# Kernel tuning notes

Hardware: AMD Instinct MI355X
Metric: run time of the kernel (lower is better)

## Reference

```python
import jax, jax.numpy as jnp
import numpy as np

B, L, HID = 2, 2048, 2048
H, KVH, HD = 8, 1, 256
GROUPS = H // KVH
THETA = 10000.0
NEG_INF = -1e9


def _rope_cos_sin(seq_len, hd):
    inv_freq = 1.0 / (THETA ** (jnp.arange(0, hd, 2, dtype=jnp.float32) / hd))
    t = jnp.arange(seq_len, dtype=jnp.float32)
    freqs = jnp.outer(t, inv_freq)                # [L, hd/2]
    emb = jnp.concatenate([freqs, freqs], axis=-1)  # [L, hd]
    return jnp.cos(emb), jnp.sin(emb)


def _rotate_half(x):
    x1, x2 = jnp.split(x, 2, axis=-1)
    return jnp.concatenate([-x2, x1], axis=-1)


def _apply_rope(x, cos, sin):
    # x: [B, h, L, hd]; cos/sin: [L, hd] broadcast over batch/heads
    return x * cos[None, None] + _rotate_half(x) * sin[None, None]


def setup_inputs() -> dict:
    key = jax.random.key(0)
    kx, kq, kk, kv, ko = jax.random.split(key, 5)
    s = lambda fan_in: 1.0 / np.sqrt(fan_in)
    x = jax.random.normal(kx, (B, L, HID), dtype=jnp.float32)
    Wq = jax.random.normal(kq, (HID, H * HD), dtype=jnp.float32) * s(HID)
    Wk = jax.random.normal(kk, (HID, KVH * HD), dtype=jnp.float32) * s(HID)
    Wv = jax.random.normal(kv, (HID, KVH * HD), dtype=jnp.float32) * s(HID)
    Wo = jax.random.normal(ko, (H * HD, HID), dtype=jnp.float32) * s(H * HD)
    # causal additive mask, same semantics as SDPA attn_mask (float, additive)
    causal = jnp.tril(jnp.ones((L, L), dtype=bool))
    mask = jnp.where(causal, 0.0, NEG_INF).astype(jnp.float32)[None, None]
    return {"x": x, "Wq": Wq, "Wk": Wk, "Wv": Wv, "Wo": Wo, "mask": mask}


def reference(x, Wq, Wk, Wv, Wo, mask):
    # projections -> [B, h, L, hd]
    q = (x @ Wq).reshape(B, L, H, HD).transpose(0, 2, 1, 3)
    k = (x @ Wk).reshape(B, L, KVH, HD).transpose(0, 2, 1, 3)
    v = (x @ Wv).reshape(B, L, KVH, HD).transpose(0, 2, 1, 3)
    cos, sin = _rope_cos_sin(L, HD)
    q = _apply_rope(q, cos, sin)
    k = _apply_rope(k, cos, sin)
    # GQA: replicate kv heads (repeat_interleave over head dim)
    k = jnp.repeat(k, GROUPS, axis=1)
    v = jnp.repeat(v, GROUPS, axis=1)
    scale = HD ** -0.5
    scores = jnp.einsum("bhqd,bhkd->bhqk", q, k) * scale + mask
    attn = jax.nn.softmax(scores.astype(jnp.float32), axis=-1).astype(q.dtype)
    out = jnp.einsum("bhqk,bhkd->bhqd", attn, v)
    out = out.transpose(0, 2, 1, 3).reshape(B, L, H * HD)
    return out @ Wo
```

## Files before the change

### kernel.cpp

```cpp
#include <hip/hip_runtime.h>

typedef unsigned short u16;
typedef __attribute__((ext_vector_type(8))) short short8x;
typedef __attribute__((ext_vector_type(4))) float f32x4;

#define B_ 2
#define L_ 2048
#define HID_ 2048
#define H_ 8
#define HD_ 256

__device__ __forceinline__ u16 f2bf(float f) {
  union { float f; unsigned u; } v; v.f = f;
  unsigned r = v.u + 0x7FFFu + ((v.u >> 16) & 1u);
  return (u16)(r >> 16);
}
__device__ __forceinline__ float bf2f(u16 u) {
  union { unsigned u; float f; } v; v.u = ((unsigned)u) << 16;
  return v.f;
}

__device__ __forceinline__ void gload_lds16(const void* g, void* l) {
  __builtin_amdgcn_global_load_lds((const __attribute__((address_space(1))) unsigned*)g,
                                   (__attribute__((address_space(3))) unsigned*)l, 16, 0, 0);
}

__global__ __launch_bounds__(256) void cvt_x_kernel(const float4* __restrict__ in,
                                                    u16* __restrict__ out) {
  int idx = blockIdx.x * 256 + threadIdx.x;
  float4 v = in[idx];
  u16* o = out + (size_t)idx * 4;
  o[0] = f2bf(v.x); o[1] = f2bf(v.y); o[2] = f2bf(v.z); o[3] = f2bf(v.w);
}

__global__ __launch_bounds__(256) void cvt_wt_kernel(const float* __restrict__ W,
                                                     u16* __restrict__ Wt, int K, int N) {
  __shared__ float tile[32][33];
  int n0 = blockIdx.x * 32, k0 = blockIdx.y * 32;
  int tx = threadIdx.x, ty = threadIdx.y;
#pragma unroll
  for (int i = 0; i < 32; i += 8)
    tile[ty + i][tx] = W[(size_t)(k0 + ty + i) * N + n0 + tx];
  __syncthreads();
#pragma unroll
  for (int i = 0; i < 32; i += 8)
    Wt[(size_t)(n0 + ty + i) * K + k0 + tx] = f2bf(tile[tx][ty + i]);
}

__global__ __launch_bounds__(256) void rope_kernel(const u16* __restrict__ in,
                                                   u16* __restrict__ out, int nh_shift,
                                                   int in_stride, int in_off, float scale) {
  int idx = blockIdx.x * 256 + threadIdx.x;
  int nh = 1 << nh_shift;
  int d = idx & 127;
  int t = idx >> 7;
  int h = t & (nh - 1);
  int row = t >> nh_shift;
  int l = row & (L_ - 1);
  int b = row >> 11;
  size_t ibase = (size_t)row * in_stride + in_off + h * 256 + d;
  float x1 = bf2f(in[ibase]);
  float x2 = bf2f(in[ibase + 128]);
  float f = exp2f(-(float)d * (13.287712379549449f / 128.0f));
  float ang = (float)l * f;
  float s, c;
  sincosf(ang, &s, &c);
  size_t obase = ((size_t)(b * nh + h) * L_ + l) * 256 + d;
  out[obase] = f2bf((x1 * c - x2 * s) * scale);
  out[obase + 128] = f2bf((x2 * c + x1 * s) * scale);
}

__global__ __launch_bounds__(256) void vt_kernel(const u16* __restrict__ qkvproj,
                                                 u16* __restrict__ vt) {
  int idx = blockIdx.x * 256 + threadIdx.x;
  int l = idx & 2047;
  int d = (idx >> 11) & 255;
  int b = idx >> 19;
  vt[idx] = qkvproj[((size_t)b * 2048 + l) * 2560 + 2304 + d];
}

template <int F32OUT>
__global__ __launch_bounds__(256) void gemm_bt_kernel(const u16* __restrict__ A,
                                                      const u16* __restrict__ Bt,
                                                      void* __restrict__ Cv,
                                                      int M, int N, int K) {
  __shared__ __attribute__((aligned(16))) u16 As[128 * 32];
  __shared__ __attribute__((aligned(16))) u16 Bs[128 * 32];
  const int tid = threadIdx.x;
  const int lane = tid & 63;
  const int w = tid >> 6;
  const int wr = w >> 1, wc = w & 1;
  const int nbx = gridDim.x;
  int flat = blockIdx.y * nbx + blockIdx.x;
  int nwg = nbx * gridDim.y;
  int q8 = nwg >> 3, r8 = nwg & 7;
  int xcd = flat & 7, idx8 = flat >> 3;
  int neu = (xcd < r8 ? xcd * (q8 + 1) : r8 * (q8 + 1) + (xcd - r8) * q8) + idx8;
  const int m0 = (neu / nbx) * 128, n0 = (neu % nbx) * 128;
  const int l15 = lane & 15, l4 = lane >> 4;
  f32x4 acc[4][4] = {};
  for (int kt = 0; kt < K; kt += 32) {
#pragma unroll
    for (int i = 0; i < 2; ++i) {
      int c = tid + i * 256;
      int row = c >> 2, cin = c & 3;
      gload_lds16(A + (size_t)(m0 + row) * K + kt + cin * 8,
                  (char*)As + (i * 256 + w * 64) * 16);
      gload_lds16(Bt + (size_t)(n0 + row) * K + kt + cin * 8,
                  (char*)Bs + (i * 256 + w * 64) * 16);
    }
    __syncthreads();
    short8x a[4], b[4];
#pragma unroll
    for (int m = 0; m < 4; ++m)
      a[m] = *(const short8x*)(&As[(wr * 64 + m * 16 + l15) * 32 + l4 * 8]);
#pragma unroll
    for (int n = 0; n < 4; ++n)
      b[n] = *(const short8x*)(&Bs[(wc * 64 + n * 16 + l15) * 32 + l4 * 8]);
#pragma unroll
    for (int m = 0; m < 4; ++m)
#pragma unroll
      for (int n = 0; n < 4; ++n)
        acc[m][n] = __builtin_amdgcn_mfma_f32_16x16x32_bf16(a[m], b[n], acc[m][n], 0, 0, 0);
    __syncthreads();
  }
#pragma unroll
  for (int m = 0; m < 4; ++m) {
#pragma unroll
    for (int n = 0; n < 4; ++n) {
      int gcol = n0 + wc * 64 + n * 16 + l15;
#pragma unroll
      for (int r = 0; r < 4; ++r) {
        int grow = m0 + wr * 64 + m * 16 + l4 * 4 + r;
        if (F32OUT)
          ((float*)Cv)[(size_t)grow * N + gcol] = acc[m][n][r];
        else
          ((u16*)Cv)[(size_t)grow * N + gcol] = f2bf(acc[m][n][r]);
      }
    }
  }
}

__global__ __launch_bounds__(256) void flash_kernel(const u16* __restrict__ qb,
                                                    const u16* __restrict__ kb,
                                                    const u16* __restrict__ vt,
                                                    u16* __restrict__ attn_o) {
  __shared__ __attribute__((aligned(16))) u16 Kbuf[2][64 * 256];
  __shared__ __attribute__((aligned(16))) u16 Vbuf[2][256 * 64];
  __shared__ __attribute__((aligned(16))) u16 Ps[4 * 16 * 64];
  const int x = blockIdx.x;
  const int j = 31 - (x >> 4);
  const int bh = x & 15;
  const int b = bh >> 3;
  const int h = bh & 7;
  const int tid = threadIdx.x, lane = tid & 63, w = tid >> 6;
  const int l15 = lane & 15, l4 = lane >> 4;
  const int q0 = j * 64 + w * 16;
  const int nt = j + 1;

  const u16* qrow = qb + ((size_t)(b * 8 + h) * L_ + q0 + l15) * 256;
  short8x qf[8];
#pragma unroll
  for (int kc = 0; kc < 8; ++kc)
    qf[kc] = *(const short8x*)(qrow + kc * 32 + l4 * 8);

  f32x4 o[16] = {};
  float mrow = -3e38f, srow = 0.f;

  const u16* kbase = kb + (size_t)b * (L_ * 256);
  const u16* vbase = vt + (size_t)b * (256 * L_);

#define STAGE(t, s)                                                            \
  {                                                                            \
    _Pragma("unroll") for (int i2 = 0; i2 < 8; ++i2) {                         \
      int c = i2 * 256 + tid;                                                  \
      int rk = c >> 5, cck = c & 31, jk = cck ^ (rk & 7);                      \
      gload_lds16(kbase + (size_t)((t) * 64 + rk) * 256 + jk * 8,              \
                  (char*)&Kbuf[s][0] + (i2 * 256 + w * 64) * 16);              \
      int rd = c >> 3, ccv = c & 7, jv = ccv ^ (rd & 7);                       \
      gload_lds16(vbase + (size_t)rd * L_ + (t) * 64 + jv * 8,                 \
                  (char*)&Vbuf[s][0] + (i2 * 256 + w * 64) * 16);              \
    }                                                                          \
  }

  STAGE(0, 0);
  asm volatile("s_waitcnt vmcnt(0)" ::: "memory");
  __syncthreads();

  for (int t = 0; t < nt; ++t) {
    if (t + 1 < nt) STAGE(t + 1, (t + 1) & 1);
    const char* Kb = (const char*)&Kbuf[t & 1][0];
    const char* Vb = (const char*)&Vbuf[t & 1][0];

    f32x4 sacc[4] = {};
    __builtin_amdgcn_s_setprio(1);
#pragma unroll
    for (int kc = 0; kc < 8; ++kc)
#pragma unroll
      for (int n = 0; n < 4; ++n) {
        int row = n * 16 + l15;
        short8x kf = *(const short8x*)(Kb +
            ((row * 512 + kc * 64 + l4 * 16) ^ ((row & 7) << 4)));
        sacc[n] = __builtin_amdgcn_mfma_f32_16x16x32_bf16(kf, qf[kc], sacc[n], 0, 0, 0);
      }
    __builtin_amdgcn_s_setprio(0);
    float p[4][4];
    const bool dm = (t == j);
    const int qg = q0 + l15;
    float pm = -3e38f;
#pragma unroll
    for (int n = 0; n < 4; ++n)
#pragma unroll
      for (int r = 0; r < 4; ++r) {
        int kvg = t * 64 + n * 16 + l4 * 4 + r;
        float v = sacc[n][r];
        if (dm && (kvg > qg)) v = -1e30f;
        p[n][r] = v;
        pm = fmaxf(pm, v);
      }
    pm = fmaxf(pm, __shfl_xor(pm, 16));
    pm = fmaxf(pm, __shfl_xor(pm, 32));
    const bool defer = __all(pm <= mrow + 8.f);
    float mn, alpha;
    if (defer) {
      mn = mrow;
    } else {
      mn = fmaxf(mrow, pm);
      alpha = __expf(mrow - mn);
      mrow = mn;
    }
    float rs = 0.f;
#pragma unroll
    for (int n = 0; n < 4; ++n)
#pragma unroll
      for (int r = 0; r < 4; ++r) {
        p[n][r] = __expf(p[n][r] - mn);
        rs += p[n][r];
      }
    rs += __shfl_xor(rs, 16);
    rs += __shfl_xor(rs, 32);
    if (defer) {
      srow += rs;
    } else {
      srow = srow * alpha + rs;
      float av[4];
#pragma unroll
      for (int r = 0; r < 4; ++r)
        av[r] = __shfl(alpha, l4 * 4 + r, 16);
#pragma unroll
      for (int ff = 0; ff < 16; ++ff) {
        o[ff][0] *= av[0]; o[ff][1] *= av[1];
        o[ff][2] *= av[2]; o[ff][3] *= av[3];
      }
    }
#pragma unroll
    for (int n = 0; n < 4; ++n)
#pragma unroll
      for (int r = 0; r < 4; r += 2) {
        unsigned pk;
        asm("v_cvt_pk_bf16_f32 %0, %1, %2" : "=v"(pk) : "v"(p[n][r]), "v"(p[n][r + 1]));
        *(unsigned*)((char*)Ps + w * 2048 +
                     ((l15 * 128 + (n * 16 + l4 * 4 + r) * 2) ^ ((l15 & 7) << 4))) = pk;
      }
    asm volatile("s_waitcnt lgkmcnt(0)" ::: "memory");
    short8x paf[2];
#pragma unroll
    for (int kc2 = 0; kc2 < 2; ++kc2)
      paf[kc2] = *(const short8x*)((const char*)Ps + w * 2048 +
          ((l15 * 128 + kc2 * 64 + l4 * 16) ^ ((l15 & 7) << 4)));
    __builtin_amdgcn_s_setprio(1);
#pragma unroll
    for (int kc2 = 0; kc2 < 2; ++kc2)
#pragma unroll
      for (int ff = 0; ff < 16; ++ff) {
        int rd = ff * 16 + l15;
        short8x vf = *(const short8x*)(Vb +
            ((rd * 128 + kc2 * 64 + l4 * 16) ^ ((rd & 7) << 4)));
        o[ff] = __builtin_amdgcn_mfma_f32_16x16x32_bf16(paf[kc2], vf, o[ff], 0, 0, 0);
      }
    __builtin_amdgcn_s_setprio(0);
    asm volatile("s_waitcnt vmcnt(0)" ::: "memory");
    __syncthreads();
  }
  float sv[4];
#pragma unroll
  for (int r = 0; r < 4; ++r)
    sv[r] = __shfl(srow, l4 * 4 + r, 16);
#pragma unroll
  for (int r = 0; r < 4; ++r) {
    float inv = 1.0f / sv[r];
    int grow = q0 + l4 * 4 + r;
    size_t base = ((size_t)b * L_ + grow) * (size_t)(H_ * HD_) + h * 256;
#pragma unroll
    for (int ff = 0; ff < 16; ++ff)
      attn_o[base + ff * 16 + l15] = f2bf(o[ff][r] * inv);
  }
#undef STAGE
}

extern "C" void kernel_launch(void* const* d_in, const int* in_sizes, int n_in,
                              void* d_out, int out_size, void* d_ws, size_t ws_size,
                              hipStream_t stream) {
  const float* x  = (const float*)d_in[0];
  const float* Wq = (const float*)d_in[1];
  const float* Wk = (const float*)d_in[2];
  const float* Wv = (const float*)d_in[3];
  const float* Wo = (const float*)d_in[4];
  float* out = (float*)d_out;
  char* ws = (char*)d_ws;
  size_t off = 0;
  auto alloc = [&](size_t bytes) {
    void* p = ws + off;
    off = (off + bytes + 255) & ~(size_t)255;
    return p;
  };
  u16* wqkv_t  = (u16*)alloc(2560ull * 2048 * 2);
  u16* wo_t    = (u16*)alloc(2048ull * 2048 * 2);
  u16* xbf     = (u16*)alloc(4096ull * 2048 * 2);
  u16* qkvproj = (u16*)alloc(4096ull * 2560 * 2);
  u16* kb      = (u16*)alloc(4096ull * 256 * 2);
  u16* vtb     = (u16*)alloc(4096ull * 256 * 2);
  u16* qbuf    = xbf;
  u16* attn_o  = qkvproj;

  cvt_x_kernel<<<8192, 256, 0, stream>>>((const float4*)x, xbf);
  cvt_wt_kernel<<<dim3(64, 64), dim3(32, 8), 0, stream>>>(Wq, wqkv_t, 2048, 2048);
  cvt_wt_kernel<<<dim3(8, 64),  dim3(32, 8), 0, stream>>>(Wk, wqkv_t + 2048ull * 2048, 2048, 256);
  cvt_wt_kernel<<<dim3(8, 64),  dim3(32, 8), 0, stream>>>(Wv, wqkv_t + 2304ull * 2048, 2048, 256);
  cvt_wt_kernel<<<dim3(64, 64), dim3(32, 8), 0, stream>>>(Wo, wo_t, 2048, 2048);

  gemm_bt_kernel<0><<<dim3(20, 32), 256, 0, stream>>>(xbf, wqkv_t, qkvproj, 4096, 2560, 2048);

  rope_kernel<<<16384, 256, 0, stream>>>(qkvproj, qbuf, 3, 2560, 0, 0.0625f);
  rope_kernel<<<2048, 256, 0, stream>>>(qkvproj, kb, 0, 2560, 2048, 1.0f);
  vt_kernel<<<4096, 256, 0, stream>>>(qkvproj, vtb);

  flash_kernel<<<512, 256, 0, stream>>>(qbuf, kb, vtb, attn_o);

  gemm_bt_kernel<1><<<dim3(16, 32), 256, 0, stream>>>(attn_o, wo_t, out, 4096, 2048, 2048);
}
```

Measured before the change: 255.1 us.

## Pair causal query tiles per block for balance; tile V transpose through LDS

The flash kernel now runs 512 threads per block. Waves 0-3 handle query tile 31-p and waves 4-7 handle tile p, and both share the staged K/V tiles. The goal is to even out causal-mask work across blocks and halve the grid while reusing each K/V load for two query tiles. In exchange, the short-tile waves sit idle at barriers once their own tile is finished, and the larger block may reduce occupancy. The V transpose kernel also switches to a 32x32 LDS tile so that both its reads and its writes are coalesced.

```diff
diff --git a/kernel.cpp b/kernel.cpp
--- a/kernel.cpp
+++ b/kernel.cpp
@@ -72,11 +72,16 @@
 
 __global__ __launch_bounds__(256) void vt_kernel(const u16* __restrict__ qkvproj,
                                                  u16* __restrict__ vt) {
-  int idx = blockIdx.x * 256 + threadIdx.x;
-  int l = idx & 2047;
-  int d = (idx >> 11) & 255;
-  int b = idx >> 19;
-  vt[idx] = qkvproj[((size_t)b * 2048 + l) * 2560 + 2304 + d];
+  __shared__ u16 tile[32][33];
+  int l0 = blockIdx.x * 32, d0 = blockIdx.y * 32, b = blockIdx.z;
+  int tx = threadIdx.x, ty = threadIdx.y;
+#pragma unroll
+  for (int i = 0; i < 32; i += 8)
+    tile[ty + i][tx] = qkvproj[((size_t)b * 2048 + l0 + ty + i) * 2560 + 2304 + d0 + tx];
+  __syncthreads();
+#pragma unroll
+  for (int i = 0; i < 32; i += 8)
+    vt[((size_t)b * 256 + d0 + ty + i) * 2048 + l0 + tx] = tile[tx][ty + i];
 }
 
 template <int F32OUT>
@@ -141,22 +146,23 @@
   }
 }
 
-__global__ __launch_bounds__(256) void flash_kernel(const u16* __restrict__ qb,
+__global__ __launch_bounds__(512) void flash_kernel(const u16* __restrict__ qb,
                                                     const u16* __restrict__ kb,
                                                     const u16* __restrict__ vt,
                                                     u16* __restrict__ attn_o) {
   __shared__ __attribute__((aligned(16))) u16 Kbuf[2][64 * 256];
   __shared__ __attribute__((aligned(16))) u16 Vbuf[2][256 * 64];
-  __shared__ __attribute__((aligned(16))) u16 Ps[4 * 16 * 64];
+  __shared__ __attribute__((aligned(16))) u16 Ps[8 * 16 * 64];
   const int x = blockIdx.x;
-  const int j = 31 - (x >> 4);
+  const int p = x >> 4;
   const int bh = x & 15;
   const int b = bh >> 3;
   const int h = bh & 7;
   const int tid = threadIdx.x, lane = tid & 63, w = tid >> 6;
   const int l15 = lane & 15, l4 = lane >> 4;
-  const int q0 = j * 64 + w * 16;
-  const int nt = j + 1;
+  const int j = (w < 4) ? (31 - p) : p;
+  const int q0 = j * 64 + (w & 3) * 16;
+  const int nt = (31 - p) + 1;
 
   const u16* qrow = qb + ((size_t)(b * 8 + h) * L_ + q0 + l15) * 256;
   short8x qf[8];
@@ -172,14 +178,14 @@
 
 #define STAGE(t, s)                                                            \
   {                                                                            \
-    _Pragma("unroll") for (int i2 = 0; i2 < 8; ++i2) {                         \
-      int c = i2 * 256 + tid;                                                  \
+    _Pragma("unroll") for (int i2 = 0; i2 < 4; ++i2) {                         \
+      int c = i2 * 512 + tid;                                                  \
       int rk = c >> 5, cck = c & 31, jk = cck ^ (rk & 7);                      \
       gload_lds16(kbase + (size_t)((t) * 64 + rk) * 256 + jk * 8,              \
-                  (char*)&Kbuf[s][0] + (i2 * 256 + w * 64) * 16);              \
+                  (char*)&Kbuf[s][0] + (i2 * 512 + w * 64) * 16);              \
       int rd = c >> 3, ccv = c & 7, jv = ccv ^ (rd & 7);                       \
       gload_lds16(vbase + (size_t)rd * L_ + (t) * 64 + jv * 8,                 \
-                  (char*)&Vbuf[s][0] + (i2 * 256 + w * 64) * 16);              \
+                  (char*)&Vbuf[s][0] + (i2 * 512 + w * 64) * 16);              \
     }                                                                          \
   }
 
@@ -189,96 +195,98 @@
 
   for (int t = 0; t < nt; ++t) {
     if (t + 1 < nt) STAGE(t + 1, (t + 1) & 1);
-    const char* Kb = (const char*)&Kbuf[t & 1][0];
-    const char* Vb = (const char*)&Vbuf[t & 1][0];
-
-    f32x4 sacc[4] = {};
-    __builtin_amdgcn_s_setprio(1);
-#pragma unroll
-    for (int kc = 0; kc < 8; ++kc)
-#pragma unroll
-      for (int n = 0; n < 4; ++n) {
-        int row = n * 16 + l15;
-        short8x kf = *(const short8x*)(Kb +
-            ((row * 512 + kc * 64 + l4 * 16) ^ ((row & 7) << 4)));
-        sacc[n] = __builtin_amdgcn_mfma_f32_16x16x32_bf16(kf, qf[kc], sacc[n], 0, 0, 0);
+    if (t <= j) {
+      const char* Kb = (const char*)&Kbuf[t & 1][0];
+      const char* Vb = (const char*)&Vbuf[t & 1][0];
+
+      f32x4 sacc[4] = {};
+      __builtin_amdgcn_s_setprio(1);
+#pragma unroll
+      for (int kc = 0; kc < 8; ++kc)
+#pragma unroll
+        for (int n = 0; n < 4; ++n) {
+          int row = n * 16 + l15;
+          short8x kf = *(const short8x*)(Kb +
+              ((row * 512 + kc * 64 + l4 * 16) ^ ((row & 7) << 4)));
+          sacc[n] = __builtin_amdgcn_mfma_f32_16x16x32_bf16(kf, qf[kc], sacc[n], 0, 0, 0);
+        }
+      __builtin_amdgcn_s_setprio(0);
+      float pp[4][4];
+      const bool dm = (t == j);
+      const int qg = q0 + l15;
+      float pm = -3e38f;
+#pragma unroll
+      for (int n = 0; n < 4; ++n)
+#pragma unroll
+        for (int r = 0; r < 4; ++r) {
+          int kvg = t * 64 + n * 16 + l4 * 4 + r;
+          float v = sacc[n][r];
+          if (dm && (kvg > qg)) v = -1e30f;
+          pp[n][r] = v;
+          pm = fmaxf(pm, v);
+        }
+      pm = fmaxf(pm, __shfl_xor(pm, 16));
+      pm = fmaxf(pm, __shfl_xor(pm, 32));
+      const bool defer = __all(pm <= mrow + 8.f);
+      float mn, alpha;
+      if (defer) {
+        mn = mrow;
+      } else {
+        mn = fmaxf(mrow, pm);
+        alpha = __expf(mrow - mn);
+        mrow = mn;
       }
-    __builtin_amdgcn_s_setprio(0);
-    float p[4][4];
-    const bool dm = (t == j);
-    const int qg = q0 + l15;
-    float pm = -3e38f;
-#pragma unroll
-    for (int n = 0; n < 4; ++n)
-#pragma unroll
-      for (int r = 0; r < 4; ++r) {
-        int kvg = t * 64 + n * 16 + l4 * 4 + r;
-        float v = sacc[n][r];
-        if (dm && (kvg > qg)) v = -1e30f;
-        p[n][r] = v;
-        pm = fmaxf(pm, v);
+      float rs = 0.f;
+#pragma unroll
+      for (int n = 0; n < 4; ++n)
+#pragma unroll
+        for (int r = 0; r < 4; ++r) {
+          pp[n][r] = __expf(pp[n][r] - mn);
+          rs += pp[n][r];
+        }
+      rs += __shfl_xor(rs, 16);
+      rs += __shfl_xor(rs, 32);
+      if (defer) {
+        srow += rs;
+      } else {
+        srow = srow * alpha + rs;
+        float av[4];
+#pragma unroll
+        for (int r = 0; r < 4; ++r)
+          av[r] = __shfl(alpha, l4 * 4 + r, 16);
+#pragma unroll
+        for (int ff = 0; ff < 16; ++ff) {
+          o[ff][0] *= av[0]; o[ff][1] *= av[1];
+          o[ff][2] *= av[2]; o[ff][3] *= av[3];
+        }
       }
-    pm = fmaxf(pm, __shfl_xor(pm, 16));
-    pm = fmaxf(pm, __shfl_xor(pm, 32));
-    const bool defer = __all(pm <= mrow + 8.f);
-    float mn, alpha;
-    if (defer) {
-      mn = mrow;
-    } else {
-      mn = fmaxf(mrow, pm);
-      alpha = __expf(mrow - mn);
-      mrow = mn;
+#pragma unroll
+      for (int n = 0; n < 4; ++n)
+#pragma unroll
+        for (int r = 0; r < 4; r += 2) {
+          unsigned pk;
+          asm("v_cvt_pk_bf16_f32 %0, %1, %2" : "=v"(pk) : "v"(pp[n][r]), "v"(pp[n][r + 1]));
+          *(unsigned*)((char*)Ps + w * 2048 +
+                       ((l15 * 128 + (n * 16 + l4 * 4 + r) * 2) ^ ((l15 & 7) << 4))) = pk;
+        }
+      asm volatile("s_waitcnt lgkmcnt(0)" ::: "memory");
+      short8x paf[2];
+#pragma unroll
+      for (int kc2 = 0; kc2 < 2; ++kc2)
+        paf[kc2] = *(const short8x*)((const char*)Ps + w * 2048 +
+            ((l15 * 128 + kc2 * 64 + l4 * 16) ^ ((l15 & 7) << 4)));
+      __builtin_amdgcn_s_setprio(1);
+#pragma unroll
+      for (int kc2 = 0; kc2 < 2; ++kc2)
+#pragma unroll
+        for (int ff = 0; ff < 16; ++ff) {
+          int rd = ff * 16 + l15;
+          short8x vf = *(const short8x*)(Vb +
+              ((rd * 128 + kc2 * 64 + l4 * 16) ^ ((rd & 7) << 4)));
+          o[ff] = __builtin_amdgcn_mfma_f32_16x16x32_bf16(paf[kc2], vf, o[ff], 0, 0, 0);
+        }
+      __builtin_amdgcn_s_setprio(0);
     }
-    float rs = 0.f;
-#pragma unroll
-    for (int n = 0; n < 4; ++n)
-#pragma unroll
-      for (int r = 0; r < 4; ++r) {
-        p[n][r] = __expf(p[n][r] - mn);
-        rs += p[n][r];
-      }
-    rs += __shfl_xor(rs, 16);
-    rs += __shfl_xor(rs, 32);
-    if (defer) {
-      srow += rs;
-    } else {
-      srow = srow * alpha + rs;
-      float av[4];
-#pragma unroll
-      for (int r = 0; r < 4; ++r)
-        av[r] = __shfl(alpha, l4 * 4 + r, 16);
-#pragma unroll
-      for (int ff = 0; ff < 16; ++ff) {
-        o[ff][0] *= av[0]; o[ff][1] *= av[1];
-        o[ff][2] *= av[2]; o[ff][3] *= av[3];
-      }
-    }
-#pragma unroll
-    for (int n = 0; n < 4; ++n)
-#pragma unroll
-      for (int r = 0; r < 4; r += 2) {
-        unsigned pk;
-        asm("v_cvt_pk_bf16_f32 %0, %1, %2" : "=v"(pk) : "v"(p[n][r]), "v"(p[n][r + 1]));
-        *(unsigned*)((char*)Ps + w * 2048 +
-                     ((l15 * 128 + (n * 16 + l4 * 4 + r) * 2) ^ ((l15 & 7) << 4))) = pk;
-      }
-    asm volatile("s_waitcnt lgkmcnt(0)" ::: "memory");
-    short8x paf[2];
-#pragma unroll
-    for (int kc2 = 0; kc2 < 2; ++kc2)
-      paf[kc2] = *(const short8x*)((const char*)Ps + w * 2048 +
-          ((l15 * 128 + kc2 * 64 + l4 * 16) ^ ((l15 & 7) << 4)));
-    __builtin_amdgcn_s_setprio(1);
-#pragma unroll
-    for (int kc2 = 0; kc2 < 2; ++kc2)
-#pragma unroll
-      for (int ff = 0; ff < 16; ++ff) {
-        int rd = ff * 16 + l15;
-        short8x vf = *(const short8x*)(Vb +
-            ((rd * 128 + kc2 * 64 + l4 * 16) ^ ((rd & 7) << 4)));
-        o[ff] = __builtin_amdgcn_mfma_f32_16x16x32_bf16(paf[kc2], vf, o[ff], 0, 0, 0);
-      }
-    __builtin_amdgcn_s_setprio(0);
     asm volatile("s_waitcnt vmcnt(0)" ::: "memory");
     __syncthreads();
   }
@@ -333,9 +341,9 @@
 
   rope_kernel<<<16384, 256, 0, stream>>>(qkvproj, qbuf, 3, 2560, 0, 0.0625f);
   rope_kernel<<<2048, 256, 0, stream>>>(qkvproj, kb, 0, 2560, 2048, 1.0f);
-  vt_kernel<<<4096, 256, 0, stream>>>(qkvproj, vtb);
-
-  flash_kernel<<<512, 256, 0, stream>>>(qbuf, kb, vtb, attn_o);
+  vt_kernel<<<dim3(64, 8, 2), dim3(32, 8), 0, stream>>>(qkvproj, vtb);
+
+  flash_kernel<<<256, 512, 0, stream>>>(qbuf, kb, vtb, attn_o);
 
   gemm_bt_kernel<1><<<dim3(16, 32), 256, 0, stream>>>(attn_o, wo_t, out, 4096, 2048, 2048);
 }
```

After: 237.1 us. 7.1% less time.
